# Optimization experiments

Measured on AMD Instinct MI355X. Metric: run time of the kernel, lower is better.

Reference implementation:

```python
import jax, jax.numpy as jnp
import numpy as np

NUM_SPLITS = 64
UNITS_PER_SPLIT = 64
IN_DIM = 4096          # divisible by NUM_SPLITS -> 64 input features per split
OUT_DIM = NUM_SPLITS * UNITS_PER_SPLIT  # 4096
BATCH = 4096
BN_EPS = 1e-3          # keras BatchNormalization default epsilon


def make_mask():
    # block_diag of NUM_SPLITS ones-blocks of shape (IN_DIM//NUM_SPLITS, UNITS_PER_SPLIT)
    din_per = IN_DIM // NUM_SPLITS
    return jnp.kron(jnp.eye(NUM_SPLITS, dtype=jnp.float32),
                    jnp.ones((din_per, UNITS_PER_SPLIT), dtype=jnp.float32))


def setup_inputs() -> dict:
    key = jax.random.key(0)
    k_x, k_w = jax.random.split(key)
    x = jax.random.normal(k_x, (BATCH, IN_DIM), dtype=jnp.float32)
    weight = jax.random.normal(k_w, (IN_DIM, OUT_DIM), dtype=jnp.float32) * (2.0 / IN_DIM) ** 0.5
    bias = jnp.full((OUT_DIM,), 0.1, dtype=jnp.float32)
    gamma = jnp.ones((OUT_DIM,), dtype=jnp.float32)
    beta = jnp.zeros((OUT_DIM,), dtype=jnp.float32)
    return {"x": x, "weight": weight, "bias": bias, "gamma": gamma, "beta": beta}


def reference(x, weight, bias, gamma, beta):
    mask = make_mask()  # [IN_DIM, OUT_DIM] block-diagonal 0/1
    # masked dense: only block-diagonal entries of weight participate
    out = jnp.matmul(x, weight * mask) + bias  # [B, OUT_DIM]
    # BatchNorm, training=True: batch statistics (biased variance), keras eps=1e-3
    mean = jnp.mean(out, axis=0)
    var = jnp.mean(jnp.square(out - mean), axis=0)
    out = (out - mean) * jax.lax.rsqrt(var + BN_EPS) * gamma + beta
    return jax.nn.relu(out)
```

## Files before the change

### kernel.cpp

```cpp
#include <hip/hip_runtime.h>
#include <hip/hip_bf16.h>

#define BATCH 4096
#define DIM 4096
#define NSPLIT 64
#define ROWS_PB 128
#define NCHUNK 32
#define BN_EPS 1e-3f

typedef __attribute__((ext_vector_type(8))) short bf16x8;
typedef __attribute__((ext_vector_type(4))) float f32x4;

__device__ inline unsigned short f2bf(float f) {
    union { float f; unsigned int u; } c; c.f = f;
    unsigned int u = c.u;
    u += 0x7FFFu + ((u >> 16) & 1u);
    return (unsigned short)(u >> 16);
}

__global__ __launch_bounds__(256) void stats_pass(
    const float* __restrict__ x, const float* __restrict__ w,
    const float* __restrict__ bias, float* __restrict__ part)
{
    __shared__ unsigned short xs[ROWS_PB][72];
    __shared__ unsigned short wt[64][72];
    __shared__ float bcol[64];
    __shared__ float red1[4][64], red2[4][64];

    const int s  = blockIdx.y;
    const int r0 = blockIdx.x * ROWS_PB;
    const int t  = threadIdx.x;
    const int lane = t & 63, wave = t >> 6;
    const int quad = lane >> 4, l16 = lane & 15;

    for (int i = t; i < 1024; i += 256) {
        int k = i >> 4, c4 = i & 15;
        float4 v = *(const float4*)(w + (size_t)(s*64 + k) * DIM + s*64 + c4*4);
        wt[c4*4 + 0][k] = f2bf(v.x);
        wt[c4*4 + 1][k] = f2bf(v.y);
        wt[c4*4 + 2][k] = f2bf(v.z);
        wt[c4*4 + 3][k] = f2bf(v.w);
    }
    if (t < 64) bcol[t] = bias[s*64 + t];

    #pragma unroll
    for (int it = 0; it < 8; it++) {
        int i = t + it * 256;
        int row = i >> 4, c4 = i & 15;
        float4 v = *(const float4*)(x + (size_t)(r0 + row) * DIM + s*64 + c4*4);
        ushort4 u;
        u.x = f2bf(v.x); u.y = f2bf(v.y); u.z = f2bf(v.z); u.w = f2bf(v.w);
        *(ushort4*)&xs[row][c4*4] = u;
    }
    __syncthreads();

    f32x4 acc[2][4];
    #pragma unroll
    for (int rt = 0; rt < 2; rt++)
        #pragma unroll
        for (int ct = 0; ct < 4; ct++) {
            float b = bcol[ct*16 + l16];
            acc[rt][ct] = (f32x4){b, b, b, b};
        }

    bf16x8 af[2][2], bf[4][2];
    #pragma unroll
    for (int rt = 0; rt < 2; rt++)
        #pragma unroll
        for (int kk = 0; kk < 2; kk++)
            af[rt][kk] = *(const bf16x8*)&xs[wave*32 + rt*16 + l16][kk*32 + quad*8];
    #pragma unroll
    for (int ct = 0; ct < 4; ct++)
        #pragma unroll
        for (int kk = 0; kk < 2; kk++)
            bf[ct][kk] = *(const bf16x8*)&wt[ct*16 + l16][kk*32 + quad*8];

    #pragma unroll
    for (int kk = 0; kk < 2; kk++)
        #pragma unroll
        for (int rt = 0; rt < 2; rt++)
            #pragma unroll
            for (int ct = 0; ct < 4; ct++)
                acc[rt][ct] = __builtin_amdgcn_mfma_f32_16x16x32_bf16(
                    af[rt][kk], bf[ct][kk], acc[rt][ct], 0, 0, 0);

    float s1[4], s2[4];
    #pragma unroll
    for (int ct = 0; ct < 4; ct++) { s1[ct] = 0.f; s2[ct] = 0.f; }
    #pragma unroll
    for (int rt = 0; rt < 2; rt++)
        #pragma unroll
        for (int ct = 0; ct < 4; ct++)
            #pragma unroll
            for (int r = 0; r < 4; r++) {
                float v = acc[rt][ct][r];
                s1[ct] += v; s2[ct] += v * v;
            }
    #pragma unroll
    for (int ct = 0; ct < 4; ct++) {
        float a = s1[ct], b = s2[ct];
        a += __shfl_xor(a, 16); b += __shfl_xor(b, 16);
        a += __shfl_xor(a, 32); b += __shfl_xor(b, 32);
        if (quad == 0) {
            red1[wave][ct*16 + l16] = a;
            red2[wave][ct*16 + l16] = b;
        }
    }
    __syncthreads();
    if (t < 64) {
        float a = red1[0][t] + red1[1][t] + red1[2][t] + red1[3][t];
        float b = red2[0][t] + red2[1][t] + red2[2][t] + red2[3][t];
        size_t base = (size_t)(s * NCHUNK + blockIdx.x) * 128;
        part[base + t]      = a;
        part[base + 64 + t] = b;
    }
}

__global__ __launch_bounds__(256) void main_pass(
    const float* __restrict__ x, const float* __restrict__ w,
    const float* __restrict__ bias, const float* __restrict__ gamma,
    const float* __restrict__ beta, const float* __restrict__ part,
    float* __restrict__ out)
{
    __shared__ unsigned short xs[ROWS_PB][72];
    __shared__ unsigned short wt[64][72];
    __shared__ float bcol[64];
    __shared__ float scol[64], shcol[64];

    const int s  = blockIdx.y;
    const int r0 = blockIdx.x * ROWS_PB;
    const int t  = threadIdx.x;
    const int lane = t & 63, wave = t >> 6;
    const int quad = lane >> 4, l16 = lane & 15;

    for (int i = t; i < 1024; i += 256) {
        int k = i >> 4, c4 = i & 15;
        float4 v = *(const float4*)(w + (size_t)(s*64 + k) * DIM + s*64 + c4*4);
        wt[c4*4 + 0][k] = f2bf(v.x);
        wt[c4*4 + 1][k] = f2bf(v.y);
        wt[c4*4 + 2][k] = f2bf(v.z);
        wt[c4*4 + 3][k] = f2bf(v.w);
    }
    if (t < 64) bcol[t] = bias[s*64 + t];

    #pragma unroll
    for (int it = 0; it < 8; it++) {
        int i = t + it * 256;
        int row = i >> 4, c4 = i & 15;
        float4 v = *(const float4*)(x + (size_t)(r0 + row) * DIM + s*64 + c4*4);
        ushort4 u;
        u.x = f2bf(v.x); u.y = f2bf(v.y); u.z = f2bf(v.z); u.w = f2bf(v.w);
        *(ushort4*)&xs[row][c4*4] = u;
    }

    if (t < 64) {
        float a = 0.f, b = 0.f;
        #pragma unroll 8
        for (int p = 0; p < NCHUNK; p++) {
            size_t base = (size_t)(s * NCHUNK + p) * 128;
            a += part[base + t];
            b += part[base + 64 + t];
        }
        float mean = a * (1.f / BATCH);
        float var  = b * (1.f / BATCH) - mean * mean;
        float rstd = rsqrtf(var + BN_EPS);
        float sc = gamma[s*64 + t] * rstd;
        scol[t]  = sc;
        shcol[t] = beta[s*64 + t] - mean * sc;
    }
    __syncthreads();

    f32x4 acc[2][4];
    #pragma unroll
    for (int rt = 0; rt < 2; rt++)
        #pragma unroll
        for (int ct = 0; ct < 4; ct++) {
            float b = bcol[ct*16 + l16];
            acc[rt][ct] = (f32x4){b, b, b, b};
        }

    bf16x8 af[2][2], bf[4][2];
    #pragma unroll
    for (int rt = 0; rt < 2; rt++)
        #pragma unroll
        for (int kk = 0; kk < 2; kk++)
            af[rt][kk] = *(const bf16x8*)&xs[wave*32 + rt*16 + l16][kk*32 + quad*8];
    #pragma unroll
    for (int ct = 0; ct < 4; ct++)
        #pragma unroll
        for (int kk = 0; kk < 2; kk++)
            bf[ct][kk] = *(const bf16x8*)&wt[ct*16 + l16][kk*32 + quad*8];

    #pragma unroll
    for (int kk = 0; kk < 2; kk++)
        #pragma unroll
        for (int rt = 0; rt < 2; rt++)
            #pragma unroll
            for (int ct = 0; ct < 4; ct++)
                acc[rt][ct] = __builtin_amdgcn_mfma_f32_16x16x32_bf16(
                    af[rt][kk], bf[ct][kk], acc[rt][ct], 0, 0, 0);

    #pragma unroll
    for (int rt = 0; rt < 2; rt++)
        #pragma unroll
        for (int ct = 0; ct < 4; ct++) {
            int col = ct*16 + l16;
            float sc = scol[col], sh = shcol[col];
            #pragma unroll
            for (int r = 0; r < 4; r++) {
                float v = fmaxf(fmaf(acc[rt][ct][r], sc, sh), 0.f);
                int row = r0 + wave*32 + rt*16 + quad*4 + r;
                out[(size_t)row * DIM + s*64 + col] = v;
            }
        }
}

extern "C" void kernel_launch(void* const* d_in, const int* in_sizes, int n_in,
                              void* d_out, int out_size, void* d_ws, size_t ws_size,
                              hipStream_t stream) {
    const float* x     = (const float*)d_in[0];
    const float* w     = (const float*)d_in[1];
    const float* bias  = (const float*)d_in[2];
    const float* gamma = (const float*)d_in[3];
    const float* beta  = (const float*)d_in[4];
    float* out  = (float*)d_out;
    float* part = (float*)d_ws;

    stats_pass<<<dim3(NCHUNK, NSPLIT), 256, 0, stream>>>(x, w, bias, part);
    main_pass<<<dim3(NCHUNK, NSPLIT), 256, 0, stream>>>(x, w, bias, gamma, beta,
                                                        part, out);
}
```

Before: 185.9 us.

## Store pre-normalized GEMM output once and apply BatchNorm in a separate elementwise pass

Instead of recomputing the block-diagonal GEMM in a second kernel, the first kernel now writes the raw GEMM result to the output buffer while also producing the per-column partial sums. A second, lightweight kernel reduces the partials and applies scale, shift and ReLU in place on the output. The bias add is dropped entirely because training-mode BatchNorm subtracts the batch mean, which cancels it. This removes the second read of x and the repeated bf16 conversion and MFMA work. In exchange it adds a full extra read and write of the 64 MB output buffer, so total memory traffic goes up.

```diff
diff --git a/kernel.cpp b/kernel.cpp
--- a/kernel.cpp
+++ b/kernel.cpp
@@ -1,5 +1,4 @@
 #include <hip/hip_runtime.h>
-#include <hip/hip_bf16.h>
 
 #define BATCH 4096
 #define DIM 4096
@@ -18,13 +17,12 @@
     return (unsigned short)(u >> 16);
 }
 
-__global__ __launch_bounds__(256) void stats_pass(
+__global__ __launch_bounds__(256) void gemm_stats(
     const float* __restrict__ x, const float* __restrict__ w,
-    const float* __restrict__ bias, float* __restrict__ part)
+    float* __restrict__ part, float* __restrict__ out)
 {
     __shared__ unsigned short xs[ROWS_PB][72];
     __shared__ unsigned short wt[64][72];
-    __shared__ float bcol[64];
     __shared__ float red1[4][64], red2[4][64];
 
     const int s  = blockIdx.y;
@@ -41,7 +39,6 @@
         wt[c4*4 + 2][k] = f2bf(v.z);
         wt[c4*4 + 3][k] = f2bf(v.w);
     }
-    if (t < 64) bcol[t] = bias[s*64 + t];
 
     #pragma unroll
     for (int it = 0; it < 8; it++) {
@@ -58,12 +55,10 @@
     #pragma unroll
     for (int rt = 0; rt < 2; rt++)
         #pragma unroll
-        for (int ct = 0; ct < 4; ct++) {
-            float b = bcol[ct*16 + l16];
-            acc[rt][ct] = (f32x4){b, b, b, b};
-        }
+        for (int ct = 0; ct < 4; ct++)
+            acc[rt][ct] = (f32x4){0.f, 0.f, 0.f, 0.f};
 
-    bf16x8 af[2][2], bf[4][2];
+    bf16x8 af[2][2], bfr[4][2];
     #pragma unroll
     for (int rt = 0; rt < 2; rt++)
         #pragma unroll
@@ -73,7 +68,7 @@
     for (int ct = 0; ct < 4; ct++)
         #pragma unroll
         for (int kk = 0; kk < 2; kk++)
-            bf[ct][kk] = *(const bf16x8*)&wt[ct*16 + l16][kk*32 + quad*8];
+            bfr[ct][kk] = *(const bf16x8*)&wt[ct*16 + l16][kk*32 + quad*8];
 
     #pragma unroll
     for (int kk = 0; kk < 2; kk++)
@@ -82,7 +77,19 @@
             #pragma unroll
             for (int ct = 0; ct < 4; ct++)
                 acc[rt][ct] = __builtin_amdgcn_mfma_f32_16x16x32_bf16(
-                    af[rt][kk], bf[ct][kk], acc[rt][ct], 0, 0, 0);
+                    af[rt][kk], bfr[ct][kk], acc[rt][ct], 0, 0, 0);
+
+    #pragma unroll
+    for (int rt = 0; rt < 2; rt++)
+        #pragma unroll
+        for (int ct = 0; ct < 4; ct++) {
+            int col = ct*16 + l16;
+            #pragma unroll
+            for (int r = 0; r < 4; r++) {
+                int row = r0 + wave*32 + rt*16 + quad*4 + r;
+                out[(size_t)row * DIM + s*64 + col] = acc[rt][ct][r];
+            }
+        }
 
     float s1[4], s2[4];
     #pragma unroll
@@ -116,42 +123,15 @@
     }
 }
 
-__global__ __launch_bounds__(256) void main_pass(
-    const float* __restrict__ x, const float* __restrict__ w,
-    const float* __restrict__ bias, const float* __restrict__ gamma,
-    const float* __restrict__ beta, const float* __restrict__ part,
-    float* __restrict__ out)
+__global__ __launch_bounds__(256) void bn_apply(
+    const float* __restrict__ part, const float* __restrict__ gamma,
+    const float* __restrict__ beta, float* __restrict__ out)
 {
-    __shared__ unsigned short xs[ROWS_PB][72];
-    __shared__ unsigned short wt[64][72];
-    __shared__ float bcol[64];
     __shared__ float scol[64], shcol[64];
 
     const int s  = blockIdx.y;
     const int r0 = blockIdx.x * ROWS_PB;
     const int t  = threadIdx.x;
-    const int lane = t & 63, wave = t >> 6;
-    const int quad = lane >> 4, l16 = lane & 15;
-
-    for (int i = t; i < 1024; i += 256) {
-        int k = i >> 4, c4 = i & 15;
-        float4 v = *(const float4*)(w + (size_t)(s*64 + k) * DIM + s*64 + c4*4);
-        wt[c4*4 + 0][k] = f2bf(v.x);
-        wt[c4*4 + 1][k] = f2bf(v.y);
-        wt[c4*4 + 2][k] = f2bf(v.z);
-        wt[c4*4 + 3][k] = f2bf(v.w);
-    }
-    if (t < 64) bcol[t] = bias[s*64 + t];
-
-    #pragma unroll
-    for (int it = 0; it < 8; it++) {
-        int i = t + it * 256;
-        int row = i >> 4, c4 = i & 15;
-        float4 v = *(const float4*)(x + (size_t)(r0 + row) * DIM + s*64 + c4*4);
-        ushort4 u;
-        u.x = f2bf(v.x); u.y = f2bf(v.y); u.z = f2bf(v.z); u.w = f2bf(v.w);
-        *(ushort4*)&xs[row][c4*4] = u;
-    }
 
     if (t < 64) {
         float a = 0.f, b = 0.f;
@@ -170,49 +150,19 @@
     }
     __syncthreads();
 
-    f32x4 acc[2][4];
     #pragma unroll
-    for (int rt = 0; rt < 2; rt++)
-        #pragma unroll
-        for (int ct = 0; ct < 4; ct++) {
-            float b = bcol[ct*16 + l16];
-            acc[rt][ct] = (f32x4){b, b, b, b};
-        }
-
-    bf16x8 af[2][2], bf[4][2];
-    #pragma unroll
-    for (int rt = 0; rt < 2; rt++)
-        #pragma unroll
-        for (int kk = 0; kk < 2; kk++)
-            af[rt][kk] = *(const bf16x8*)&xs[wave*32 + rt*16 + l16][kk*32 + quad*8];
-    #pragma unroll
-    for (int ct = 0; ct < 4; ct++)
-        #pragma unroll
-        for (int kk = 0; kk < 2; kk++)
-            bf[ct][kk] = *(const bf16x8*)&wt[ct*16 + l16][kk*32 + quad*8];
-
-    #pragma unroll
-    for (int kk = 0; kk < 2; kk++)
-        #pragma unroll
-        for (int rt = 0; rt < 2; rt++)
-            #pragma unroll
-            for (int ct = 0; ct < 4; ct++)
-                acc[rt][ct] = __builtin_amdgcn_mfma_f32_16x16x32_bf16(
-                    af[rt][kk], bf[ct][kk], acc[rt][ct], 0, 0, 0);
-
-    #pragma unroll
-    for (int rt = 0; rt < 2; rt++)
-        #pragma unroll
-        for (int ct = 0; ct < 4; ct++) {
-            int col = ct*16 + l16;
-            float sc = scol[col], sh = shcol[col];
-            #pragma unroll
-            for (int r = 0; r < 4; r++) {
-                float v = fmaxf(fmaf(acc[rt][ct][r], sc, sh), 0.f);
-                int row = r0 + wave*32 + rt*16 + quad*4 + r;
-                out[(size_t)row * DIM + s*64 + col] = v;
-            }
-        }
+    for (int it = 0; it < 8; it++) {
+        int i = t + it * 256;
+        int row = i >> 4, c4 = i & 15;
+        float* p = out + (size_t)(r0 + row) * DIM + s*64 + c4*4;
+        float4 v = *(const float4*)p;
+        int c0 = c4*4;
+        v.x = fmaxf(fmaf(v.x, scol[c0+0], shcol[c0+0]), 0.f);
+        v.y = fmaxf(fmaf(v.y, scol[c0+1], shcol[c0+1]), 0.f);
+        v.z = fmaxf(fmaf(v.z, scol[c0+2], shcol[c0+2]), 0.f);
+        v.w = fmaxf(fmaf(v.w, scol[c0+3], shcol[c0+3]), 0.f);
+        *(float4*)p = v;
+    }
 }
 
 extern "C" void kernel_launch(void* const* d_in, const int* in_sizes, int n_in,
@@ -220,13 +170,11 @@
                               hipStream_t stream) {
     const float* x     = (const float*)d_in[0];
     const float* w     = (const float*)d_in[1];
-    const float* bias  = (const float*)d_in[2];
     const float* gamma = (const float*)d_in[3];
     const float* beta  = (const float*)d_in[4];
     float* out  = (float*)d_out;
     float* part = (float*)d_ws;
 
-    stats_pass<<<dim3(NCHUNK, NSPLIT), 256, 0, stream>>>(x, w, bias, part);
-    main_pass<<<dim3(NCHUNK, NSPLIT), 256, 0, stream>>>(x, w, bias, gamma, beta,
-                                                        part, out);
+    gemm_stats<<<dim3(NCHUNK, NSPLIT), 256, 0, stream>>>(x, w, part, out);
+    bn_apply<<<dim3(NCHUNK, NSPLIT), 256, 0, stream>>>(part, gamma, beta, out);
 }
```

After: 185.2 us. Within noise of the previous version (-0.4%).
